# Optimization experiments

Hardware: AMD Instinct MI355X
Metric: run time of the kernel (lower is better)

## Reference

```python
import jax, jax.numpy as jnp
import numpy as np

B, S, H, E = 2, 2048, 1024, 16


def setup_inputs() -> dict:
    key = jax.random.key(0)
    k0, k1, k2, k3 = jax.random.split(key, 4)
    tokens = jax.random.normal(k0, (B, S, H), dtype=jnp.float32)
    gate_w = jax.random.normal(k1, (E, H), dtype=jnp.float32) * (H ** -0.5)
    expert_w = jax.random.normal(k2, (E, H, H), dtype=jnp.float32) * (H ** -0.5)
    expert_b = jax.random.normal(k3, (E, H), dtype=jnp.float32) * 0.01
    return {"tokens": tokens, "gate_w": gate_w, "expert_w": expert_w, "expert_b": expert_b}


def reference(tokens, gate_w, expert_w, expert_b):
    b, s, h = tokens.shape
    # gate: Linear(H, E, bias=False) -> logits, softmax, top-2
    logits = jnp.einsum('bsh,eh->bse', tokens, gate_w)
    weights = jax.nn.softmax(logits, axis=-1)
    top2_w, top2_idx = jax.lax.top_k(weights, 2)           # [b,s,2]
    flat = tokens.reshape(b * s, h)                         # [N,H]
    flat_w = top2_w.reshape(b * s, 2)
    flat_idx = top2_idx.reshape(b * s, 2)
    # dense per-expert Linear+ReLU for all tokens (grouped GEMM form)
    y = jax.nn.relu(jnp.einsum('nh,edh->ned', flat, expert_w) + expert_b[None, :, :])  # [N,E,H]
    # gather the two selected experts per token and combine with gate weights
    sel = jnp.take_along_axis(y, flat_idx[:, :, None], axis=1)  # [N,2,H]
    out = jnp.sum(sel * flat_w[:, :, None], axis=1)             # [N,H]
    return out.reshape(b, s, h)
```

## Files before the change

### kernel.cpp

```cpp
#include <hip/hip_runtime.h>
#include <hip/hip_bf16.h>

#define TOKENS 4096
#define HDIM 1024
#define NEXP 16
#define BM 128
#define BN 128
#define BK 64
#define MAX_TILES (TOKENS * 2 / BM + NEXP)

typedef __bf16 bf16x8 __attribute__((ext_vector_type(8)));
typedef float f32x4 __attribute__((ext_vector_type(4)));

__device__ inline void gload16(const void* g, const void* l) {
  __builtin_amdgcn_global_load_lds((const __attribute__((address_space(1))) void*)g,
                                   (__attribute__((address_space(3))) void*)l, 16, 0, 0);
}

__global__ __launch_bounds__(256) void cvt_kernel(const float* __restrict__ src,
                                                  __bf16* __restrict__ dst) {
  int i = blockIdx.x * 256 + threadIdx.x;
  float4 a = ((const float4*)src)[i * 2];
  float4 b = ((const float4*)src)[i * 2 + 1];
  bf16x8 v;
  v[0] = (__bf16)a.x; v[1] = (__bf16)a.y; v[2] = (__bf16)a.z; v[3] = (__bf16)a.w;
  v[4] = (__bf16)b.x; v[5] = (__bf16)b.y; v[6] = (__bf16)b.z; v[7] = (__bf16)b.w;
  ((bf16x8*)dst)[i] = v;
}

__global__ __launch_bounds__(256) void gate_kernel(
    const float* __restrict__ tokens, const float* __restrict__ gate_w,
    int* __restrict__ tok_idx, float* __restrict__ tok_w) {
  int lane = threadIdx.x & 63;
  int wv = threadIdx.x >> 6;
  int token = blockIdx.x * 4 + wv;
  const float* trow = tokens + (size_t)token * HDIM;

  float4 tv[4];
#pragma unroll
  for (int s = 0; s < 4; ++s) tv[s] = *(const float4*)(trow + s * 256 + lane * 4);

  float lg[NEXP];
#pragma unroll
  for (int e = 0; e < NEXP; ++e) {
    float d = 0.f;
#pragma unroll
    for (int s = 0; s < 4; ++s) {
      float4 g = *(const float4*)(gate_w + e * HDIM + s * 256 + lane * 4);
      d += tv[s].x * g.x + tv[s].y * g.y + tv[s].z * g.z + tv[s].w * g.w;
    }
#pragma unroll
    for (int off = 32; off; off >>= 1) d += __shfl_xor(d, off);
    lg[e] = d;
  }

  int i0 = 0; float b0 = lg[0];
#pragma unroll
  for (int e = 1; e < NEXP; ++e) if (lg[e] > b0) { b0 = lg[e]; i0 = e; }
  int i1 = -1; float b1 = -1e30f;
#pragma unroll
  for (int e = 0; e < NEXP; ++e) {
    if (e == i0) continue;
    if (lg[e] > b1) { b1 = lg[e]; i1 = e; }
  }
  float s = 0.f;
#pragma unroll
  for (int e = 0; e < NEXP; ++e) s += expf(lg[e] - b0);
  float w0 = 1.0f / s;
  float w1 = expf(b1 - b0) / s;

  if (lane == 0) {
    tok_idx[token * 2 + 0] = i0;
    tok_idx[token * 2 + 1] = i1;
    tok_w[token * 2 + 0] = w0;
    tok_w[token * 2 + 1] = w1;
  }
}

__global__ __launch_bounds__(256) void build_lists_kernel(
    const int* __restrict__ tok_idx, const float* __restrict__ tok_w,
    int* __restrict__ counts, int* __restrict__ list_tok, float* __restrict__ list_w) {
  int e = blockIdx.x;
  __shared__ int cur;
  if (threadIdx.x == 0) cur = 0;
  __syncthreads();
  for (int s = threadIdx.x; s < TOKENS * 2; s += 256) {
    if (tok_idx[s] == e) {
      int pos = atomicAdd(&cur, 1);
      list_tok[e * TOKENS + pos] = s >> 1;
      list_w[e * TOKENS + pos] = tok_w[s];
    }
  }
  __syncthreads();
  if (threadIdx.x == 0) counts[e] = cur;
}

__global__ void plan_kernel(const int* __restrict__ counts, int* __restrict__ tiles,
                            int* __restrict__ n_tiles) {
  if (threadIdx.x == 0) {
    int n = 0;
    for (int e = 0; e < NEXP; ++e) {
      int t = (counts[e] + BM - 1) / BM;
      for (int m = 0; m < t; ++m) { tiles[n * 2] = e; tiles[n * 2 + 1] = m; ++n; }
    }
    *n_tiles = n;
  }
}

__global__ __launch_bounds__(512, 4) void moe_gemm_kernel(
    const __bf16* __restrict__ tok_bf, const __bf16* __restrict__ w_bf,
    const float* __restrict__ expert_b, const int* __restrict__ counts,
    const int* __restrict__ tiles, const int* __restrict__ n_tiles,
    const int* __restrict__ list_tok, const float* __restrict__ list_w,
    float* __restrict__ out) {
  int bx = blockIdx.x;
  if (bx >= *n_tiles) return;
  int e = tiles[bx * 2];
  int mt = tiles[bx * 2 + 1];
  int cnt = counts[e];
  int nt = blockIdx.y;
  const int lbase = e * TOKENS;

  __shared__ __bf16 lds[2][(BM + BN) * BK];

  int tid = threadIdx.x;
  int lane = tid & 63;
  int wv = tid >> 6;

  const __bf16* aptr[2];
  const __bf16* bptr[2];
  int dstb[2];
#pragma unroll
  for (int i = 0; i < 2; ++i) {
    int c = (wv * 2 + i) * 64 + lane;
    int r = c >> 3, kc = c & 7;
    int gr = mt * BM + r;
    int tok = list_tok[lbase + ((gr < cnt) ? gr : (cnt - 1))];
    aptr[i] = tok_bf + (size_t)tok * HDIM + (kc ^ (r & 7)) * 8;
    int d = nt * BN + r;
    bptr[i] = w_bf + (size_t)e * HDIM * HDIM + (size_t)d * HDIM + (kc ^ (r & 7)) * 8;
    dstb[i] = (wv * 2 + i) * 512;
  }

  int wr = (wv >> 2) * 64;
  int wc = (wv & 3) * 32;
  int lr = lane & 15;
  int lk = lane >> 4;

  int aoffr[2][4], boffr[2][2];
#pragma unroll
  for (int kk = 0; kk < 2; ++kk) {
#pragma unroll
    for (int m = 0; m < 4; ++m) {
      int r = wr + m * 16 + lr;
      aoffr[kk][m] = r * BK + (((kk * 4 + lk) ^ (r & 7)) * 8);
    }
#pragma unroll
    for (int n = 0; n < 2; ++n) {
      int d = wc + n * 16 + lr;
      boffr[kk][n] = BM * BK + d * BK + (((kk * 4 + lk) ^ (d & 7)) * 8);
    }
  }

  f32x4 acc[4][2] = {};

#pragma unroll
  for (int i = 0; i < 2; ++i) gload16(aptr[i], &lds[0][dstb[i]]);
#pragma unroll
  for (int i = 0; i < 2; ++i) gload16(bptr[i], &lds[0][BM * BK + dstb[i]]);
  __syncthreads();

  int buf = 0;
  for (int kb = 0; kb < HDIM / BK; ++kb) {
    if (kb + 1 < HDIM / BK) {
      int nb = buf ^ 1;
      int ko = (kb + 1) * BK;
#pragma unroll
      for (int i = 0; i < 2; ++i) gload16(aptr[i] + ko, &lds[nb][dstb[i]]);
#pragma unroll
      for (int i = 0; i < 2; ++i) gload16(bptr[i] + ko, &lds[nb][BM * BK + dstb[i]]);
    }

    bf16x8 af[2][4], bfr[2][2];
#pragma unroll
    for (int kk = 0; kk < 2; ++kk) {
#pragma unroll
      for (int m = 0; m < 4; ++m) af[kk][m] = *(const bf16x8*)(&lds[buf][aoffr[kk][m]]);
#pragma unroll
      for (int n = 0; n < 2; ++n) bfr[kk][n] = *(const bf16x8*)(&lds[buf][boffr[kk][n]]);
    }
#pragma unroll
    for (int kk = 0; kk < 2; ++kk)
#pragma unroll
      for (int m = 0; m < 4; ++m)
#pragma unroll
        for (int n = 0; n < 2; ++n)
          acc[m][n] = __builtin_amdgcn_mfma_f32_16x16x32_bf16(af[kk][m], bfr[kk][n], acc[m][n], 0, 0, 0);

    __syncthreads();
    buf ^= 1;
  }

#pragma unroll
  for (int m = 0; m < 4; ++m) {
#pragma unroll
    for (int j = 0; j < 4; ++j) {
      int rloc = wr + m * 16 + lk * 4 + j;
      int grow = mt * BM + rloc;
      if (grow < cnt) {
        int tok = list_tok[lbase + grow];
        float gw = list_w[lbase + grow];
        float* orow = out + (size_t)tok * HDIM + nt * BN + wc;
        const float* brow = expert_b + e * HDIM + nt * BN + wc;
#pragma unroll
        for (int n = 0; n < 2; ++n) {
          int dcol = n * 16 + lr;
          float v = acc[m][n][j] + brow[dcol];
          v = fmaxf(v, 0.f) * gw;
          atomicAdd(orow + dcol, v);
        }
      }
    }
  }
}

extern "C" void kernel_launch(void* const* d_in, const int* in_sizes, int n_in,
                              void* d_out, int out_size, void* d_ws, size_t ws_size,
                              hipStream_t stream) {
  const float* tokens = (const float*)d_in[0];
  const float* gate_w = (const float*)d_in[1];
  const float* expert_w = (const float*)d_in[2];
  const float* expert_b = (const float*)d_in[3];
  float* out = (float*)d_out;

  int* counts = (int*)d_ws;
  int* n_tiles = counts + 16;
  int* tiles = n_tiles + 16;
  int* tok_idx = tiles + MAX_TILES * 2;
  float* tok_w = (float*)(tok_idx + TOKENS * 2);
  int* list_tok = (int*)(tok_w + TOKENS * 2);
  float* list_w = (float*)(list_tok + NEXP * TOKENS);
  size_t head = (size_t)(list_w + NEXP * TOKENS) - (size_t)d_ws;
  head = (head + 255) & ~(size_t)255;
  __bf16* w_bf = (__bf16*)((char*)d_ws + head);
  __bf16* tok_bf = w_bf + (size_t)NEXP * HDIM * HDIM;

  hipMemsetAsync(d_out, 0, (size_t)out_size * sizeof(float), stream);

  cvt_kernel<<<NEXP * HDIM * HDIM / 8 / 256, 256, 0, stream>>>(expert_w, w_bf);
  cvt_kernel<<<TOKENS * HDIM / 8 / 256, 256, 0, stream>>>(tokens, tok_bf);
  gate_kernel<<<TOKENS / 4, 256, 0, stream>>>(tokens, gate_w, tok_idx, tok_w);
  build_lists_kernel<<<NEXP, 256, 0, stream>>>(tok_idx, tok_w, counts, list_tok, list_w);
  plan_kernel<<<1, 64, 0, stream>>>(counts, tiles, n_tiles);

  dim3 grid(MAX_TILES, HDIM / BN);
  moe_gemm_kernel<<<grid, 512, 0, stream>>>(tok_bf, w_bf, expert_b, counts, tiles, n_tiles,
                                            list_tok, list_w, out);
}
```

Before: 227.7 us.

## Fuse all MoE stages into one persistent kernel with grid barriers

```diff
diff --git a/kernel.cpp b/kernel.cpp
--- a/kernel.cpp
+++ b/kernel.cpp
@@ -7,7 +7,8 @@
 #define BM 128
 #define BN 128
 #define BK 64
-#define MAX_TILES (TOKENS * 2 / BM + NEXP)
+#define NBLK 512
+#define NTHR 512
 
 typedef __bf16 bf16x8 __attribute__((ext_vector_type(8)));
 typedef float f32x4 __attribute__((ext_vector_type(4)));
@@ -17,209 +18,240 @@
                                    (__attribute__((address_space(3))) void*)l, 16, 0, 0);
 }
 
-__global__ __launch_bounds__(256) void cvt_kernel(const float* __restrict__ src,
-                                                  __bf16* __restrict__ dst) {
-  int i = blockIdx.x * 256 + threadIdx.x;
-  float4 a = ((const float4*)src)[i * 2];
-  float4 b = ((const float4*)src)[i * 2 + 1];
-  bf16x8 v;
-  v[0] = (__bf16)a.x; v[1] = (__bf16)a.y; v[2] = (__bf16)a.z; v[3] = (__bf16)a.w;
-  v[4] = (__bf16)b.x; v[5] = (__bf16)b.y; v[6] = (__bf16)b.z; v[7] = (__bf16)b.w;
-  ((bf16x8*)dst)[i] = v;
-}
-
-__global__ __launch_bounds__(256) void gate_kernel(
+__device__ inline void grid_barrier(int* bar, int gen) {
+  __syncthreads();
+  if (threadIdx.x == 0) {
+    __threadfence();
+    if (atomicAdd(&bar[0], 1) == NBLK - 1) {
+      atomicExch(&bar[0], 0);
+      __threadfence();
+      atomicAdd(&bar[1], 1);
+    } else {
+      while (atomicAdd(&bar[1], 0) < gen) __builtin_amdgcn_s_sleep(8);
+    }
+    __threadfence();
+  }
+  __syncthreads();
+}
+
+__global__ __launch_bounds__(NTHR, 4) void moe_fused(
     const float* __restrict__ tokens, const float* __restrict__ gate_w,
-    int* __restrict__ tok_idx, float* __restrict__ tok_w) {
-  int lane = threadIdx.x & 63;
-  int wv = threadIdx.x >> 6;
-  int token = blockIdx.x * 4 + wv;
-  const float* trow = tokens + (size_t)token * HDIM;
-
-  float4 tv[4];
-#pragma unroll
-  for (int s = 0; s < 4; ++s) tv[s] = *(const float4*)(trow + s * 256 + lane * 4);
-
-  float lg[NEXP];
-#pragma unroll
-  for (int e = 0; e < NEXP; ++e) {
-    float d = 0.f;
-#pragma unroll
-    for (int s = 0; s < 4; ++s) {
-      float4 g = *(const float4*)(gate_w + e * HDIM + s * 256 + lane * 4);
-      d += tv[s].x * g.x + tv[s].y * g.y + tv[s].z * g.z + tv[s].w * g.w;
-    }
-#pragma unroll
-    for (int off = 32; off; off >>= 1) d += __shfl_xor(d, off);
-    lg[e] = d;
-  }
-
-  int i0 = 0; float b0 = lg[0];
-#pragma unroll
-  for (int e = 1; e < NEXP; ++e) if (lg[e] > b0) { b0 = lg[e]; i0 = e; }
-  int i1 = -1; float b1 = -1e30f;
-#pragma unroll
-  for (int e = 0; e < NEXP; ++e) {
-    if (e == i0) continue;
-    if (lg[e] > b1) { b1 = lg[e]; i1 = e; }
-  }
-  float s = 0.f;
-#pragma unroll
-  for (int e = 0; e < NEXP; ++e) s += expf(lg[e] - b0);
-  float w0 = 1.0f / s;
-  float w1 = expf(b1 - b0) / s;
-
-  if (lane == 0) {
-    tok_idx[token * 2 + 0] = i0;
-    tok_idx[token * 2 + 1] = i1;
-    tok_w[token * 2 + 0] = w0;
-    tok_w[token * 2 + 1] = w1;
-  }
-}
-
-__global__ __launch_bounds__(256) void build_lists_kernel(
-    const int* __restrict__ tok_idx, const float* __restrict__ tok_w,
-    int* __restrict__ counts, int* __restrict__ list_tok, float* __restrict__ list_w) {
-  int e = blockIdx.x;
-  __shared__ int cur;
-  if (threadIdx.x == 0) cur = 0;
-  __syncthreads();
-  for (int s = threadIdx.x; s < TOKENS * 2; s += 256) {
-    if (tok_idx[s] == e) {
-      int pos = atomicAdd(&cur, 1);
-      list_tok[e * TOKENS + pos] = s >> 1;
-      list_w[e * TOKENS + pos] = tok_w[s];
-    }
-  }
-  __syncthreads();
-  if (threadIdx.x == 0) counts[e] = cur;
-}
-
-__global__ void plan_kernel(const int* __restrict__ counts, int* __restrict__ tiles,
-                            int* __restrict__ n_tiles) {
-  if (threadIdx.x == 0) {
-    int n = 0;
-    for (int e = 0; e < NEXP; ++e) {
-      int t = (counts[e] + BM - 1) / BM;
-      for (int m = 0; m < t; ++m) { tiles[n * 2] = e; tiles[n * 2 + 1] = m; ++n; }
-    }
-    *n_tiles = n;
-  }
-}
-
-__global__ __launch_bounds__(512, 4) void moe_gemm_kernel(
-    const __bf16* __restrict__ tok_bf, const __bf16* __restrict__ w_bf,
-    const float* __restrict__ expert_b, const int* __restrict__ counts,
-    const int* __restrict__ tiles, const int* __restrict__ n_tiles,
-    const int* __restrict__ list_tok, const float* __restrict__ list_w,
-    float* __restrict__ out) {
-  int bx = blockIdx.x;
-  if (bx >= *n_tiles) return;
-  int e = tiles[bx * 2];
-  int mt = tiles[bx * 2 + 1];
-  int cnt = counts[e];
-  int nt = blockIdx.y;
-  const int lbase = e * TOKENS;
-
+    const float* __restrict__ expert_w, const float* __restrict__ expert_b,
+    float* __restrict__ out, int* __restrict__ bar,
+    int* __restrict__ tok_idx, float* __restrict__ tok_w,
+    int* __restrict__ counts, int* __restrict__ list_tok, float* __restrict__ list_w,
+    int* __restrict__ tiles, int* __restrict__ n_tiles_g,
+    __bf16* __restrict__ w_bf, __bf16* __restrict__ tok_bf) {
   __shared__ __bf16 lds[2][(BM + BN) * BK];
+  __shared__ int s_cur;
+  __shared__ int s_h[NEXP];
 
   int tid = threadIdx.x;
   int lane = tid & 63;
   int wv = tid >> 6;
-
-  const __bf16* aptr[2];
-  const __bf16* bptr[2];
-  int dstb[2];
-#pragma unroll
-  for (int i = 0; i < 2; ++i) {
-    int c = (wv * 2 + i) * 64 + lane;
-    int r = c >> 3, kc = c & 7;
-    int gr = mt * BM + r;
-    int tok = list_tok[lbase + ((gr < cnt) ? gr : (cnt - 1))];
-    aptr[i] = tok_bf + (size_t)tok * HDIM + (kc ^ (r & 7)) * 8;
-    int d = nt * BN + r;
-    bptr[i] = w_bf + (size_t)e * HDIM * HDIM + (size_t)d * HDIM + (kc ^ (r & 7)) * 8;
-    dstb[i] = (wv * 2 + i) * 512;
-  }
-
-  int wr = (wv >> 2) * 64;
-  int wc = (wv & 3) * 32;
-  int lr = lane & 15;
-  int lk = lane >> 4;
-
-  int aoffr[2][4], boffr[2][2];
-#pragma unroll
-  for (int kk = 0; kk < 2; ++kk) {
-#pragma unroll
-    for (int m = 0; m < 4; ++m) {
-      int r = wr + m * 16 + lr;
-      aoffr[kk][m] = r * BK + (((kk * 4 + lk) ^ (r & 7)) * 8);
-    }
-#pragma unroll
-    for (int n = 0; n < 2; ++n) {
-      int d = wc + n * 16 + lr;
-      boffr[kk][n] = BM * BK + d * BK + (((kk * 4 + lk) ^ (d & 7)) * 8);
-    }
-  }
-
-  f32x4 acc[4][2] = {};
-
-#pragma unroll
-  for (int i = 0; i < 2; ++i) gload16(aptr[i], &lds[0][dstb[i]]);
-#pragma unroll
-  for (int i = 0; i < 2; ++i) gload16(bptr[i], &lds[0][BM * BK + dstb[i]]);
-  __syncthreads();
-
-  int buf = 0;
-  for (int kb = 0; kb < HDIM / BK; ++kb) {
-    if (kb + 1 < HDIM / BK) {
-      int nb = buf ^ 1;
-      int ko = (kb + 1) * BK;
-#pragma unroll
-      for (int i = 0; i < 2; ++i) gload16(aptr[i] + ko, &lds[nb][dstb[i]]);
-#pragma unroll
-      for (int i = 0; i < 2; ++i) gload16(bptr[i] + ko, &lds[nb][BM * BK + dstb[i]]);
-    }
-
-    bf16x8 af[2][4], bfr[2][2];
+  int bid = blockIdx.x;
+
+  {
+    size_t gtid = (size_t)bid * NTHR + tid;
+    size_t gs = (size_t)NBLK * NTHR;
+    float4* out4 = (float4*)out;
+    for (size_t i = gtid; i < (size_t)TOKENS * HDIM / 4; i += gs)
+      out4[i] = float4{0.f, 0.f, 0.f, 0.f};
+    const float4* w4 = (const float4*)expert_w;
+    bf16x8* wb8 = (bf16x8*)w_bf;
+    for (size_t i = gtid; i < (size_t)NEXP * HDIM * HDIM / 8; i += gs) {
+      float4 a = w4[2 * i], b = w4[2 * i + 1];
+      bf16x8 v;
+      v[0] = (__bf16)a.x; v[1] = (__bf16)a.y; v[2] = (__bf16)a.z; v[3] = (__bf16)a.w;
+      v[4] = (__bf16)b.x; v[5] = (__bf16)b.y; v[6] = (__bf16)b.z; v[7] = (__bf16)b.w;
+      wb8[i] = v;
+    }
+    const float4* t4 = (const float4*)tokens;
+    bf16x8* tb8 = (bf16x8*)tok_bf;
+    for (size_t i = gtid; i < (size_t)TOKENS * HDIM / 8; i += gs) {
+      float4 a = t4[2 * i], b = t4[2 * i + 1];
+      bf16x8 v;
+      v[0] = (__bf16)a.x; v[1] = (__bf16)a.y; v[2] = (__bf16)a.z; v[3] = (__bf16)a.w;
+      v[4] = (__bf16)b.x; v[5] = (__bf16)b.y; v[6] = (__bf16)b.z; v[7] = (__bf16)b.w;
+      tb8[i] = v;
+    }
+  }
+
+  {
+    int token = bid * 8 + wv;
+    const float* trow = tokens + (size_t)token * HDIM;
+    float4 tv[4];
+#pragma unroll
+    for (int s = 0; s < 4; ++s) tv[s] = *(const float4*)(trow + s * 256 + lane * 4);
+    float lg[NEXP];
+#pragma unroll
+    for (int e = 0; e < NEXP; ++e) {
+      float d = 0.f;
+#pragma unroll
+      for (int s = 0; s < 4; ++s) {
+        float4 g = *(const float4*)(gate_w + e * HDIM + s * 256 + lane * 4);
+        d += tv[s].x * g.x + tv[s].y * g.y + tv[s].z * g.z + tv[s].w * g.w;
+      }
+#pragma unroll
+      for (int off = 32; off; off >>= 1) d += __shfl_xor(d, off);
+      lg[e] = d;
+    }
+    int i0 = 0; float b0 = lg[0];
+#pragma unroll
+    for (int e = 1; e < NEXP; ++e) if (lg[e] > b0) { b0 = lg[e]; i0 = e; }
+    int i1 = -1; float b1 = -1e30f;
+#pragma unroll
+    for (int e = 0; e < NEXP; ++e) {
+      if (e == i0) continue;
+      if (lg[e] > b1) { b1 = lg[e]; i1 = e; }
+    }
+    float s = 0.f;
+#pragma unroll
+    for (int e = 0; e < NEXP; ++e) s += expf(lg[e] - b0);
+    if (lane == 0) {
+      tok_idx[token * 2 + 0] = i0;
+      tok_idx[token * 2 + 1] = i1;
+      tok_w[token * 2 + 0] = 1.0f / s;
+      tok_w[token * 2 + 1] = expf(b1 - b0) / s;
+    }
+  }
+
+  grid_barrier(bar, 1);
+
+  if (bid < NEXP) {
+    if (tid == 0) s_cur = 0;
+    __syncthreads();
+    for (int s = tid; s < TOKENS * 2; s += NTHR) {
+      if (tok_idx[s] == bid) {
+        int pos = atomicAdd(&s_cur, 1);
+        list_tok[bid * TOKENS + pos] = s >> 1;
+        list_w[bid * TOKENS + pos] = tok_w[s];
+      }
+    }
+    __syncthreads();
+    if (tid == 0) counts[bid] = s_cur;
+  } else if (bid == NEXP) {
+    if (tid < NEXP) s_h[tid] = 0;
+    __syncthreads();
+    for (int s = tid; s < TOKENS * 2; s += NTHR) atomicAdd(&s_h[tok_idx[s]], 1);
+    __syncthreads();
+    if (tid == 0) {
+      int n = 0;
+      for (int e = 0; e < NEXP; ++e) {
+        int tcnt = (s_h[e] + BM - 1) >> 7;
+        for (int m = 0; m < tcnt; ++m) { tiles[2 * n] = e; tiles[2 * n + 1] = m; ++n; }
+      }
+      *n_tiles_g = n * 8;
+    }
+  }
+
+  grid_barrier(bar, 2);
+
+  {
+    int n_tiles = *n_tiles_g;
+    int lr = lane & 15;
+    int lk = lane >> 4;
+    int wr = (wv >> 2) * 64;
+    int wc = (wv & 3) * 32;
+
+    int dstb[2];
+#pragma unroll
+    for (int i = 0; i < 2; ++i) dstb[i] = (wv * 2 + i) * 512;
+
+    int aoffr[2][4], boffr[2][2];
 #pragma unroll
     for (int kk = 0; kk < 2; ++kk) {
 #pragma unroll
-      for (int m = 0; m < 4; ++m) af[kk][m] = *(const bf16x8*)(&lds[buf][aoffr[kk][m]]);
-#pragma unroll
-      for (int n = 0; n < 2; ++n) bfr[kk][n] = *(const bf16x8*)(&lds[buf][boffr[kk][n]]);
-    }
-#pragma unroll
-    for (int kk = 0; kk < 2; ++kk)
-#pragma unroll
-      for (int m = 0; m < 4; ++m)
-#pragma unroll
-        for (int n = 0; n < 2; ++n)
-          acc[m][n] = __builtin_amdgcn_mfma_f32_16x16x32_bf16(af[kk][m], bfr[kk][n], acc[m][n], 0, 0, 0);
-
-    __syncthreads();
-    buf ^= 1;
-  }
-
-#pragma unroll
-  for (int m = 0; m < 4; ++m) {
-#pragma unroll
-    for (int j = 0; j < 4; ++j) {
-      int rloc = wr + m * 16 + lk * 4 + j;
-      int grow = mt * BM + rloc;
-      if (grow < cnt) {
-        int tok = list_tok[lbase + grow];
-        float gw = list_w[lbase + grow];
-        float* orow = out + (size_t)tok * HDIM + nt * BN + wc;
-        const float* brow = expert_b + e * HDIM + nt * BN + wc;
-#pragma unroll
-        for (int n = 0; n < 2; ++n) {
-          int dcol = n * 16 + lr;
-          float v = acc[m][n][j] + brow[dcol];
-          v = fmaxf(v, 0.f) * gw;
-          atomicAdd(orow + dcol, v);
+      for (int m = 0; m < 4; ++m) {
+        int r = wr + m * 16 + lr;
+        aoffr[kk][m] = r * BK + (((kk * 4 + lk) ^ (r & 7)) * 8);
+      }
+#pragma unroll
+      for (int n = 0; n < 2; ++n) {
+        int d = wc + n * 16 + lr;
+        boffr[kk][n] = BM * BK + d * BK + (((kk * 4 + lk) ^ (d & 7)) * 8);
+      }
+    }
+
+    for (int t = bid; t < n_tiles; t += NBLK) {
+      int pair = t >> 3, nt = t & 7;
+      int e = tiles[2 * pair], mt = tiles[2 * pair + 1];
+      int cnt = counts[e];
+      int lbase = e * TOKENS;
+
+      const __bf16* aptr[2];
+      const __bf16* bptr[2];
+#pragma unroll
+      for (int i = 0; i < 2; ++i) {
+        int c = (wv * 2 + i) * 64 + lane;
+        int r = c >> 3, kc = c & 7;
+        int gr = mt * BM + r;
+        int tok = list_tok[lbase + min(gr, cnt - 1)];
+        aptr[i] = tok_bf + (size_t)tok * HDIM + (kc ^ (r & 7)) * 8;
+        int d = nt * BN + r;
+        bptr[i] = w_bf + ((size_t)e * HDIM + d) * HDIM + (kc ^ (r & 7)) * 8;
+      }
+
+      f32x4 acc[4][2] = {};
+
+#pragma unroll
+      for (int i = 0; i < 2; ++i) gload16(aptr[i], &lds[0][dstb[i]]);
+#pragma unroll
+      for (int i = 0; i < 2; ++i) gload16(bptr[i], &lds[0][BM * BK + dstb[i]]);
+      __syncthreads();
+
+      int buf = 0;
+      for (int kb = 0; kb < HDIM / BK; ++kb) {
+        if (kb + 1 < HDIM / BK) {
+          int nb = buf ^ 1;
+          int ko = (kb + 1) * BK;
+#pragma unroll
+          for (int i = 0; i < 2; ++i) gload16(aptr[i] + ko, &lds[nb][dstb[i]]);
+#pragma unroll
+          for (int i = 0; i < 2; ++i) gload16(bptr[i] + ko, &lds[nb][BM * BK + dstb[i]]);
         }
-      }
+
+        bf16x8 af[2][4], bfr[2][2];
+#pragma unroll
+        for (int kk = 0; kk < 2; ++kk) {
+#pragma unroll
+          for (int m = 0; m < 4; ++m) af[kk][m] = *(const bf16x8*)(&lds[buf][aoffr[kk][m]]);
+#pragma unroll
+          for (int n = 0; n < 2; ++n) bfr[kk][n] = *(const bf16x8*)(&lds[buf][boffr[kk][n]]);
+        }
+#pragma unroll
+        for (int kk = 0; kk < 2; ++kk)
+#pragma unroll
+          for (int m = 0; m < 4; ++m)
+#pragma unroll
+            for (int n = 0; n < 2; ++n)
+              acc[m][n] = __builtin_amdgcn_mfma_f32_16x16x32_bf16(af[kk][m], bfr[kk][n], acc[m][n], 0, 0, 0);
+
+        __syncthreads();
+        buf ^= 1;
+      }
+
+#pragma unroll
+      for (int m = 0; m < 4; ++m) {
+#pragma unroll
+        for (int j = 0; j < 4; ++j) {
+          int rloc = wr + m * 16 + lk * 4 + j;
+          int grow = mt * BM + rloc;
+          if (grow < cnt) {
+            int tok = list_tok[lbase + grow];
+            float gw = list_w[lbase + grow];
+            float* orow = out + (size_t)tok * HDIM + nt * BN + wc;
+            const float* brow = expert_b + e * HDIM + nt * BN + wc;
+#pragma unroll
+            for (int n = 0; n < 2; ++n) {
+              int dc = n * 16 + lr;
+              float v = acc[m][n][j] + brow[dc];
+              atomicAdd(orow + dc, fmaxf(v, 0.f) * gw);
+            }
+          }
+        }
+      }
+      __syncthreads();
     }
   }
 }
@@ -233,10 +265,11 @@
   const float* expert_b = (const float*)d_in[3];
   float* out = (float*)d_out;
 
-  int* counts = (int*)d_ws;
-  int* n_tiles = counts + 16;
-  int* tiles = n_tiles + 16;
-  int* tok_idx = tiles + MAX_TILES * 2;
+  int* bar = (int*)d_ws;
+  int* counts = bar + 16;
+  int* n_tiles_g = counts + 16;
+  int* tiles = n_tiles_g + 16;
+  int* tok_idx = tiles + 192;
   float* tok_w = (float*)(tok_idx + TOKENS * 2);
   int* list_tok = (int*)(tok_w + TOKENS * 2);
   float* list_w = (float*)(list_tok + NEXP * TOKENS);
@@ -245,15 +278,9 @@
   __bf16* w_bf = (__bf16*)((char*)d_ws + head);
   __bf16* tok_bf = w_bf + (size_t)NEXP * HDIM * HDIM;
 
-  hipMemsetAsync(d_out, 0, (size_t)out_size * sizeof(float), stream);
-
-  cvt_kernel<<<NEXP * HDIM * HDIM / 8 / 256, 256, 0, stream>>>(expert_w, w_bf);
-  cvt_kernel<<<TOKENS * HDIM / 8 / 256, 256, 0, stream>>>(tokens, tok_bf);
-  gate_kernel<<<TOKENS / 4, 256, 0, stream>>>(tokens, gate_w, tok_idx, tok_w);
-  build_lists_kernel<<<NEXP, 256, 0, stream>>>(tok_idx, tok_w, counts, list_tok, list_w);
-  plan_kernel<<<1, 64, 0, stream>>>(counts, tiles, n_tiles);
-
-  dim3 grid(MAX_TILES, HDIM / BN);
-  moe_gemm_kernel<<<grid, 512, 0, stream>>>(tok_bf, w_bf, expert_b, counts, tiles, n_tiles,
-                                            list_tok, list_w, out);
-}
+  hipMemsetAsync(bar, 0, 2 * sizeof(int), stream);
+
+  moe_fused<<<NBLK, NTHR, 0, stream>>>(tokens, gate_w, expert_w, expert_b, out, bar,
+                                       tok_idx, tok_w, counts, list_tok, list_w,
+                                       tiles, n_tiles_g, w_bf, tok_bf);
+}
```

New measurement: 284.6 us. 25.0% more time.
